# Optimization experiments

Hardware: AMD Instinct MI355X
Metric: run time of the kernel (lower is better)

The kernel has to match this reference:

```python
import jax, jax.numpy as jnp
import numpy as np

B, T, D, H = 32, 512, 512, 8
DH = D // H
NEG = -(2.0 ** 32) + 1.0  # matches torch's (-2**32 + 1) padding value
EPS = 1e-8


def setup_inputs() -> dict:
    key = jax.random.key(0)
    ks = jax.random.split(key, 10)
    s = 1.0 / np.sqrt(D)
    return {
        "queries": jax.random.normal(ks[0], (B, T, D), jnp.float32),
        "keys": jax.random.normal(ks[1], (B, T, D), jnp.float32),
        "Wq": jax.random.normal(ks[2], (D, D), jnp.float32) * s,
        "bq": jnp.zeros((D,), jnp.float32),
        "Wk": jax.random.normal(ks[3], (D, D), jnp.float32) * s,
        "bk": jnp.zeros((D,), jnp.float32),
        "Wv": jax.random.normal(ks[4], (D, D), jnp.float32) * s,
        "bv": jnp.zeros((D,), jnp.float32),
        "gamma": jnp.ones((D,), jnp.float32),
        "beta": jnp.zeros((D,), jnp.float32),
    }


def reference(queries, keys, Wq, bq, Wk, bk, Wv, bv, gamma, beta):
    b, tq, d = queries.shape
    tk = keys.shape[1]
    # projections (torch Linear: x @ W.T + b)
    Q = (queries @ Wq.T + bq).reshape(b, tq, H, DH)
    K = (keys @ Wk.T + bk).reshape(b, tk, H, DH)
    V = (keys @ Wv.T + bv).reshape(b, tk, H, DH)
    # scaled scores: [b, h, tq, tk]
    scores = jnp.einsum("bqhd,bkhd->bhqk", Q, K) / np.float32(np.sqrt(DH))
    # key padding mask (1 where key row sum != 0)
    key_mask = jnp.sign(jnp.abs(keys.sum(-1)))  # [b, tk]
    scores = jnp.where(key_mask[:, None, None, :] == 0, NEG, scores)
    # causal mask
    tril = jnp.tril(jnp.ones((tq, tk), scores.dtype))
    scores = jnp.where(tril[None, None, :, :] == 0, NEG, scores)
    attn = jax.nn.softmax(scores, axis=-1)  # [b, h, tq, tk]
    # query padding mask (zeros out rows for padded queries)
    query_mask = jnp.sign(jnp.abs(queries.sum(-1)))  # [b, tq]
    attn_m = attn * query_mask[:, None, :, None]
    # (dropout_rate == 0 -> identity)
    out = jnp.einsum("bhqk,bkhd->bqhd", attn_m, V).reshape(b, tq, d)
    # residual + LayerNorm (torch .std() is unbiased, ddof=1; eps added to std)
    x = out + queries
    mean = x.mean(-1, keepdims=True)
    std = jnp.std(x, axis=-1, ddof=1, keepdims=True)
    y = gamma * (x - mean) / (std + EPS) + beta
    return y
```

## Files before the change

kernel.cpp:

```cpp
#include <hip/hip_runtime.h>
#include <hip/hip_bf16.h>
#include <math.h>

#define B 32
#define T 512
#define D 512
#define H 8
#define DH 64
#define NEGV (-4294967295.0f)
#define LN_EPS 1e-8f

typedef __attribute__((ext_vector_type(8))) short bf16x8;
typedef __attribute__((ext_vector_type(4))) float f32x4;

__device__ inline f32x4 mfma16(bf16x8 a, bf16x8 b, f32x4 c) {
    return __builtin_amdgcn_mfma_f32_16x16x32_bf16(a, b, c, 0, 0, 0);
}

__device__ inline float fexp2(float x) { return __builtin_amdgcn_exp2f(x); }

#define GLDS16(g, l)                                                      \
    __builtin_amdgcn_global_load_lds(                                     \
        (const __attribute__((address_space(1))) void*)(g),               \
        (__attribute__((address_space(3))) void*)(l), 16, 0, 0)

__device__ inline unsigned short bf16bits(float x) {
    __hip_bfloat16 h = __float2bfloat16(x);
    union { __hip_bfloat16 h; unsigned short u; } cv;
    cv.h = h;
    return cv.u;
}

__device__ inline float b2f(unsigned short u) {
    union { unsigned u; float f; } c;
    c.u = ((unsigned)u) << 16;
    return c.f;
}

__global__ __launch_bounds__(256) void convert_all(
    const float* __restrict__ queries, const float* __restrict__ keys,
    const float* __restrict__ Wq, const float* __restrict__ Wk,
    const float* __restrict__ Wv,
    __hip_bfloat16* __restrict__ Qx, __hip_bfloat16* __restrict__ Kx,
    __hip_bfloat16* __restrict__ Wbf,
    float* __restrict__ qmask, float* __restrict__ kmask)
{
    const int tid = threadIdx.x;
    if (blockIdx.x >= 4096) {
        const int i = (blockIdx.x - 4096) * 2 + blockIdx.y;
        const int mat = i >> 7;
        const float* Ws = (mat == 0) ? Wq : (mat == 1) ? Wk : Wv;
        const int idx = ((i & 127) * 256 + tid) * 8;
        float4 a = *(const float4*)&Ws[idx];
        float4 c = *(const float4*)&Ws[idx + 4];
        union { unsigned short u[8]; bf16x8 v; } pk;
        pk.u[0] = bf16bits(a.x); pk.u[1] = bf16bits(a.y);
        pk.u[2] = bf16bits(a.z); pk.u[3] = bf16bits(a.w);
        pk.u[4] = bf16bits(c.x); pk.u[5] = bf16bits(c.y);
        pk.u[6] = bf16bits(c.z); pk.u[7] = bf16bits(c.w);
        *(bf16x8*)&Wbf[(size_t)mat * 262144 + idx] = pk.v;
        return;
    }

    const int wid = tid >> 6;
    const int lane = tid & 63;
    const int row = blockIdx.x * 4 + wid;
    const float* src = blockIdx.y ? keys : queries;
    __hip_bfloat16* dst = blockIdx.y ? Kx : Qx;
    float* dm = blockIdx.y ? kmask : qmask;

    const float4* p = (const float4*)(src + (size_t)row * 512);
    float4 a = p[lane * 2];
    float4 c = p[lane * 2 + 1];
    float s = a.x + a.y + a.z + a.w + c.x + c.y + c.z + c.w;

    union { unsigned short u[8]; bf16x8 v; } pk;
    pk.u[0] = bf16bits(a.x); pk.u[1] = bf16bits(a.y);
    pk.u[2] = bf16bits(a.z); pk.u[3] = bf16bits(a.w);
    pk.u[4] = bf16bits(c.x); pk.u[5] = bf16bits(c.y);
    pk.u[6] = bf16bits(c.z); pk.u[7] = bf16bits(c.w);
    *(bf16x8*)&dst[(size_t)row * 512 + lane * 8] = pk.v;

#pragma unroll
    for (int off = 32; off > 0; off >>= 1) s += __shfl_xor(s, off, 64);
    if (lane == 0)
        dm[row] = blockIdx.y ? ((s != 0.0f) ? 0.0f : NEGV)
                             : ((s != 0.0f) ? 1.0f : 0.0f);
}

__global__ __launch_bounds__(256) void qkv_qk(
    const __hip_bfloat16* __restrict__ Qx, const __hip_bfloat16* __restrict__ Kx,
    const __hip_bfloat16* __restrict__ Wbf,
    const float* __restrict__ bq, const float* __restrict__ bk,
    __hip_bfloat16* __restrict__ Qbf, __hip_bfloat16* __restrict__ Kbf)
{
    const int mat = blockIdx.z;
    const __hip_bfloat16* X  = mat ? Kx : Qx;
    const __hip_bfloat16* Wm = Wbf + (size_t)mat * 262144;
    const float* bias = mat ? bk : bq;
    __hip_bfloat16* Out = mat ? Kbf : Qbf;
    const float sc = mat ? 1.0f : 0.18033688011112042f;

    const int bm = blockIdx.x * 128;
    const int bn = blockIdx.y * 128;
    const int tid = threadIdx.x;
    const int w = tid >> 6, lane = tid & 63;
    const int lo = lane & 15, hi = lane >> 4;
    const int wm = (w >> 1) * 64, wn = (w & 1) * 64;

    __shared__ __hip_bfloat16 As[2][128 * 32];
    __shared__ __hip_bfloat16 Bs[2][128 * 32];

    const int r0 = tid >> 2,          g0 = (tid & 3) ^ ((r0 >> 1) & 3);
    const int r1 = (tid + 256) >> 2,  g1 = ((tid + 256) & 3) ^ ((r1 >> 1) & 3);
    const __hip_bfloat16* sA0 = X  + (size_t)(bm + r0) * 512 + g0 * 8;
    const __hip_bfloat16* sA1 = X  + (size_t)(bm + r1) * 512 + g1 * 8;
    const __hip_bfloat16* sB0 = Wm + (size_t)(bn + r0) * 512 + g0 * 8;
    const __hip_bfloat16* sB1 = Wm + (size_t)(bn + r1) * 512 + g1 * 8;
    const int dst0 = (w * 64) * 8;
    const int dst1 = (256 + w * 64) * 8;

    int offA[4], offB[4];
#pragma unroll
    for (int mi = 0; mi < 4; ++mi) {
        int r = wm + mi * 16 + lo;
        offA[mi] = r * 32 + ((hi ^ ((r >> 1) & 3)) * 8);
    }
#pragma unroll
    for (int ni = 0; ni < 4; ++ni) {
        int r = wn + ni * 16 + lo;
        offB[ni] = r * 32 + ((hi ^ ((r >> 1) & 3)) * 8);
    }

    f32x4 acc[4][4];
#pragma unroll
    for (int mi = 0; mi < 4; ++mi)
#pragma unroll
        for (int ni = 0; ni < 4; ++ni)
            acc[mi][ni] = (f32x4){0.f, 0.f, 0.f, 0.f};

    GLDS16(sA0, &As[0][dst0]);
    GLDS16(sA1, &As[0][dst1]);
    GLDS16(sB0, &Bs[0][dst0]);
    GLDS16(sB1, &Bs[0][dst1]);
    __syncthreads();

    for (int kt = 0; kt < 16; ++kt) {
        const int cur = kt & 1;
        if (kt < 15) {
            const int k0 = (kt + 1) * 32;
            GLDS16(sA0 + k0, &As[cur ^ 1][dst0]);
            GLDS16(sA1 + k0, &As[cur ^ 1][dst1]);
            GLDS16(sB0 + k0, &Bs[cur ^ 1][dst0]);
            GLDS16(sB1 + k0, &Bs[cur ^ 1][dst1]);
        }
        bf16x8 af[4], bfr[4];
#pragma unroll
        for (int mi = 0; mi < 4; ++mi) af[mi]  = *(const bf16x8*)&As[cur][offA[mi]];
#pragma unroll
        for (int ni = 0; ni < 4; ++ni) bfr[ni] = *(const bf16x8*)&Bs[cur][offB[ni]];
#pragma unroll
        for (int mi = 0; mi < 4; ++mi)
#pragma unroll
            for (int ni = 0; ni < 4; ++ni)
                acc[mi][ni] = mfma16(bfr[ni], af[mi], acc[mi][ni]);
        __syncthreads();
    }

    float4 b4[4];
#pragma unroll
    for (int ni = 0; ni < 4; ++ni)
        b4[ni] = *(const float4*)&bias[bn + wn + ni * 16 + hi * 4];
#pragma unroll
    for (int mi = 0; mi < 4; ++mi) {
        const size_t tok = bm + wm + mi * 16 + lo;
        __hip_bfloat16* orow = Out + tok * 512 + bn + wn + hi * 4;
#pragma unroll
        for (int ni = 0; ni < 4; ++ni) {
            union { ushort4 u4; unsigned short us[4]; } pk;
            pk.us[0] = bf16bits((acc[mi][ni][0] + b4[ni].x) * sc);
            pk.us[1] = bf16bits((acc[mi][ni][1] + b4[ni].y) * sc);
            pk.us[2] = bf16bits((acc[mi][ni][2] + b4[ni].z) * sc);
            pk.us[3] = bf16bits((acc[mi][ni][3] + b4[ni].w) * sc);
            *(ushort4*)(orow + ni * 16) = pk.u4;
        }
    }
}

__global__ __launch_bounds__(256) void qkv_v(
    const __hip_bfloat16* __restrict__ Kx, const __hip_bfloat16* __restrict__ Wbf,
    const float* __restrict__ bv, __hip_bfloat16* __restrict__ Vtb)
{
    const __hip_bfloat16* X  = Kx;
    const __hip_bfloat16* Wm = Wbf + (size_t)2 * 262144;
    const float* bias = bv;

    const int bm = blockIdx.x * 128;
    const int bn = blockIdx.y * 128;
    const int tid = threadIdx.x;
    const int w = tid >> 6, lane = tid & 63;
    const int lo = lane & 15, hi = lane >> 4;
    const int wm = (w >> 1) * 64, wn = (w & 1) * 64;

    __shared__ __hip_bfloat16 As[2][128 * 32];
    __shared__ __hip_bfloat16 Bs[2][128 * 32];

    const int r0 = tid >> 2,          g0 = (tid & 3) ^ ((r0 >> 1) & 3);
    const int r1 = (tid + 256) >> 2,  g1 = ((tid + 256) & 3) ^ ((r1 >> 1) & 3);
    const __hip_bfloat16* sA0 = X  + (size_t)(bm + r0) * 512 + g0 * 8;
    const __hip_bfloat16* sA1 = X  + (size_t)(bm + r1) * 512 + g1 * 8;
    const __hip_bfloat16* sB0 = Wm + (size_t)(bn + r0) * 512 + g0 * 8;
    const __hip_bfloat16* sB1 = Wm + (size_t)(bn + r1) * 512 + g1 * 8;
    const int dst0 = (w * 64) * 8;
    const int dst1 = (256 + w * 64) * 8;

    int offA[4], offB[4];
#pragma unroll
    for (int mi = 0; mi < 4; ++mi) {
        int r = wm + mi * 16 + lo;
        offA[mi] = r * 32 + ((hi ^ ((r >> 1) & 3)) * 8);
    }
#pragma unroll
    for (int ni = 0; ni < 4; ++ni) {
        int r = wn + ni * 16 + lo;
        offB[ni] = r * 32 + ((hi ^ ((r >> 1) & 3)) * 8);
    }

    f32x4 acc[4][4];
#pragma unroll
    for (int mi = 0; mi < 4; ++mi)
#pragma unroll
        for (int ni = 0; ni < 4; ++ni)
            acc[mi][ni] = (f32x4){0.f, 0.f, 0.f, 0.f};

    GLDS16(sA0, &As[0][dst0]);
    GLDS16(sA1, &As[0][dst1]);
    GLDS16(sB0, &Bs[0][dst0]);
    GLDS16(sB1, &Bs[0][dst1]);
    __syncthreads();

    for (int kt = 0; kt < 16; ++kt) {
        const int cur = kt & 1;
        if (kt < 15) {
            const int k0 = (kt + 1) * 32;
            GLDS16(sA0 + k0, &As[cur ^ 1][dst0]);
            GLDS16(sA1 + k0, &As[cur ^ 1][dst1]);
            GLDS16(sB0 + k0, &Bs[cur ^ 1][dst0]);
            GLDS16(sB1 + k0, &Bs[cur ^ 1][dst1]);
        }
        bf16x8 af[4], bfr[4];
#pragma unroll
        for (int mi = 0; mi < 4; ++mi) af[mi]  = *(const bf16x8*)&As[cur][offA[mi]];
#pragma unroll
        for (int ni = 0; ni < 4; ++ni) bfr[ni] = *(const bf16x8*)&Bs[cur][offB[ni]];
#pragma unroll
        for (int mi = 0; mi < 4; ++mi)
#pragma unroll
            for (int ni = 0; ni < 4; ++ni)
                acc[mi][ni] = mfma16(af[mi], bfr[ni], acc[mi][ni]);
        __syncthreads();
    }

    float bcol[4];
#pragma unroll
    for (int ni = 0; ni < 4; ++ni) bcol[ni] = bias[bn + wn + ni * 16 + lo];
    const int bb = bm >> 9;
    const int tb = (bm & 511) + wm;
#pragma unroll
    for (int ni = 0; ni < 4; ++ni) {
        const int n = bn + wn + ni * 16 + lo;
        const int hh = n >> 6, dh = n & 63;
#pragma unroll
        for (int mi = 0; mi < 4; ++mi) {
            const int tok = tb + mi * 16 + hi * 4;
            const int ktl = tok >> 6, tl = tok & 63;
            union { ushort4 u4; unsigned short us[4]; } pk;
#pragma unroll
            for (int j = 0; j < 4; ++j)
                pk.us[j] = bf16bits(acc[mi][ni][j] + bcol[ni]);
            *(ushort4*)(Vtb + ((((size_t)(bb * 8 + hh) * 8 + ktl) * 64 + dh) * 64 + tl))
                = pk.u4;
        }
    }
}

__global__ __launch_bounds__(256, 4) void flash_attn(
    const __hip_bfloat16* __restrict__ Qbf, const __hip_bfloat16* __restrict__ Kbf,
    const __hip_bfloat16* __restrict__ Vtb, const float* __restrict__ qmask,
    const float* __restrict__ kmneg, __hip_bfloat16* __restrict__ Oattn)
{
    const int flat = blockIdx.x + (blockIdx.y << 2) + (blockIdx.z << 5);
    const int rm = ((flat & 7) << 7) + (flat >> 3);
    const int pr = rm & 3;
    const int h  = (rm >> 2) & 7;
    const int b  = rm >> 5;

    const int tid  = threadIdx.x;
    const int w    = tid >> 6;
    const int lane = tid & 63;
    const int lo = lane & 15;
    const int hi = lane >> 4;

    __shared__ __hip_bfloat16 Ks[2][4096];
    __shared__ __hip_bfloat16 p_lds[4][16][72];

    const float* km = kmneg + b * T;
    const __hip_bfloat16* Kh = Kbf + (size_t)b * T * D + h * DH;
    const __hip_bfloat16* Vh = Vtb + (size_t)(b * H + h) * T * DH;

    const int sr0 = tid >> 3,         sg0 = (tid & 7) ^ (sr0 & 7);
    const int sr1 = (tid + 256) >> 3, sg1 = ((tid + 256) & 7) ^ (sr1 & 7);
    const __hip_bfloat16* sK0 = Kh + (size_t)sr0 * 512 + sg0 * 8;
    const __hip_bfloat16* sK1 = Kh + (size_t)sr1 * 512 + sg1 * 8;
    __hip_bfloat16* dK0a = &Ks[0][w * 512];
    __hip_bfloat16* dK0b = &Ks[0][2048 + w * 512];
    __hip_bfloat16* dK1a = &Ks[1][w * 512];
    __hip_bfloat16* dK1b = &Ks[1][2048 + w * 512];

#define STAGEK(bufp, kt) do {                                              \
        const size_t _o = (size_t)(kt) * 32768;                            \
        GLDS16(sK0 + _o, (bufp) ? dK1a : dK0a);                            \
        GLDS16(sK1 + _o, (bufp) ? dK1b : dK0b);                            \
    } while (0)

    int kfoff[4][2];
#pragma unroll
    for (int c = 0; c < 4; ++c)
#pragma unroll
        for (int j = 0; j < 2; ++j)
            kfoff[c][j] = (c * 16 + lo) * 64 + (((j * 4 + hi) ^ (lo & 7)) * 8);

    f32x4 cb[4];
#pragma unroll
    for (int c = 0; c < 4; ++c)
#pragma unroll
        for (int j = 0; j < 4; ++j)
            cb[c][j] = (c * 16 + hi * 4 + j <= w * 16 + lo) ? 0.0f : NEGV;

    const int nt1 = pr + 1;

    int qtile = pr;
    int q = qtile * 64 + w * 16 + lo;
    const __hip_bfloat16* Qrow = Qbf + (size_t)(b * T + q) * D + h * DH;
    bf16x8 qf0 = *(const bf16x8*)(Qrow + hi * 8);
    bf16x8 qf1 = *(const bf16x8*)(Qrow + 32 + hi * 8);

    f32x4 o[4];
    float mrun = -INFINITY, lrun = 0.f;
#pragma unroll
    for (int d = 0; d < 4; ++d) o[d] = (f32x4){0.f, 0.f, 0.f, 0.f};

    STAGEK(0, 0);

    for (int i = 0; i < 9; ++i) {
        const int cur = i & 1;
        const bool diag = (i == nt1 - 1) || (i == 8);
        if (i < 8) {
            const int nxt = (i + 1 < nt1) ? (i + 1) : (i + 1 - nt1);
            STAGEK(cur ^ 1, nxt);
            asm volatile("s_waitcnt vmcnt(2)" ::: "memory");
        } else {
            asm volatile("s_waitcnt vmcnt(0)" ::: "memory");
        }
        __builtin_amdgcn_s_barrier();
        __builtin_amdgcn_sched_barrier(0);

        if (i == nt1) {
            const float inv = qmask[b * T + q] / lrun;
            __hip_bfloat16* orow = Oattn + (size_t)(b * T + q) * D + h * DH;
#pragma unroll
            for (int db = 0; db < 4; ++db) {
                union { ushort4 u4; unsigned short us[4]; } pk;
#pragma unroll
                for (int j = 0; j < 4; ++j)
                    pk.us[j] = bf16bits(o[db][j] * inv);
                *(ushort4*)(orow + db * 16 + hi * 4) = pk.u4;
            }
            qtile = 7 - pr;
            q = qtile * 64 + w * 16 + lo;
            const __hip_bfloat16* Qrow2 = Qbf + (size_t)(b * T + q) * D + h * DH;
            qf0 = *(const bf16x8*)(Qrow2 + hi * 8);
            qf1 = *(const bf16x8*)(Qrow2 + 32 + hi * 8);
            mrun = -INFINITY; lrun = 0.f;
#pragma unroll
            for (int d = 0; d < 4; ++d) o[d] = (f32x4){0.f, 0.f, 0.f, 0.f};
        }

        const int kt = (i < nt1) ? i : (i - nt1);
        const int kb = kt * 64;

        const __hip_bfloat16* Vtile = Vh + (size_t)kt * 4096;
        bf16x8 vf[4][2];
#pragma unroll
        for (int db = 0; db < 4; ++db) {
            const __hip_bfloat16* Vrow = Vtile + (db * 16 + lo) * 64;
            vf[db][0] = *(const bf16x8*)(Vrow + hi * 8);
            vf[db][1] = *(const bf16x8*)(Vrow + 32 + hi * 8);
        }

        bf16x8 kf[4][2];
#pragma unroll
        for (int c = 0; c < 4; ++c) {
            kf[c][0] = *(const bf16x8*)&Ks[cur][kfoff[c][0]];
            kf[c][1] = *(const bf16x8*)&Ks[cur][kfoff[c][1]];
        }

        f32x4 S[4];
#pragma unroll
        for (int c = 0; c < 4; ++c) {
            f32x4 acc = (f32x4){0.f, 0.f, 0.f, 0.f};
            acc = mfma16(kf[c][0], qf0, acc);
            acc = mfma16(kf[c][1], qf1, acc);
            acc += *(const f32x4*)(km + kb + c * 16 + hi * 4);
            if (diag) acc += cb[c];
            S[c] = acc;
        }

        float tm0 = fmaxf(fmaxf(S[0][0], S[0][1]), fmaxf(S[0][2], S[0][3]));
        float tm1 = fmaxf(fmaxf(S[1][0], S[1][1]), fmaxf(S[1][2], S[1][3]));
        float tm2 = fmaxf(fmaxf(S[2][0], S[2][1]), fmaxf(S[2][2], S[2][3]));
        float tm3 = fmaxf(fmaxf(S[3][0], S[3][1]), fmaxf(S[3][2], S[3][3]));
        float tm = fmaxf(fmaxf(tm0, tm1), fmaxf(tm2, tm3));
        tm = fmaxf(tm, __shfl_xor(tm, 16, 64));
        tm = fmaxf(tm, __shfl_xor(tm, 32, 64));

        const float nm = fmaxf(mrun, tm);
        const float alpha = fexp2(mrun - nm);
        mrun = nm;
#pragma unroll
        for (int d = 0; d < 4; ++d)
#pragma unroll
            for (int j = 0; j < 4; ++j)
                o[d][j] *= alpha;

        float ps = 0.f;
#pragma unroll
        for (int c = 0; c < 4; ++c) {
            union { ushort4 u4; unsigned short us[4]; } pk;
#pragma unroll
            for (int j = 0; j < 4; ++j) {
                float p = fexp2(S[c][j] - nm);
                ps += p;
                pk.us[j] = bf16bits(p);
            }
            *(ushort4*)&p_lds[w][lo][c * 16 + hi * 4] = pk.u4;
        }
        ps += __shfl_xor(ps, 16, 64);
        ps += __shfl_xor(ps, 32, 64);
        lrun = lrun * alpha + ps;

        asm volatile("s_waitcnt lgkmcnt(0)" ::: "memory");
        __builtin_amdgcn_sched_barrier(0);

#pragma unroll
        for (int half = 0; half < 2; ++half) {
            bf16x8 pf = *(const bf16x8*)&p_lds[w][lo][half * 32 + hi * 8];
#pragma unroll
            for (int db = 0; db < 4; ++db)
                o[db] = mfma16(vf[db][half], pf, o[db]);
        }

        __builtin_amdgcn_s_barrier();
    }

    {
        const float inv = qmask[b * T + q] / lrun;
        __hip_bfloat16* orow = Oattn + (size_t)(b * T + q) * D + h * DH;
#pragma unroll
        for (int db = 0; db < 4; ++db) {
            union { ushort4 u4; unsigned short us[4]; } pk;
#pragma unroll
            for (int j = 0; j < 4; ++j)
                pk.us[j] = bf16bits(o[db][j] * inv);
            *(ushort4*)(orow + db * 16 + hi * 4) = pk.u4;
        }
    }
#undef STAGEK
}

__global__ __launch_bounds__(256) void resid_ln(
    const __hip_bfloat16* __restrict__ Oa, const float* __restrict__ queries,
    const float* __restrict__ gamma, const float* __restrict__ beta,
    float* __restrict__ out)
{
    const int w = threadIdx.x >> 6;
    const int lane = threadIdx.x & 63;
    const int row = blockIdx.x * 4 + w;
    const size_t base = (size_t)row * 512 + lane * 8;

    bf16x8 oa = *(const bf16x8*)((const unsigned short*)Oa + base);
    float4 q0 = *(const float4*)(queries + base);
    float4 q1 = *(const float4*)(queries + base + 4);

    float x[8];
    x[0] = b2f((unsigned short)oa[0]) + q0.x;
    x[1] = b2f((unsigned short)oa[1]) + q0.y;
    x[2] = b2f((unsigned short)oa[2]) + q0.z;
    x[3] = b2f((unsigned short)oa[3]) + q0.w;
    x[4] = b2f((unsigned short)oa[4]) + q1.x;
    x[5] = b2f((unsigned short)oa[5]) + q1.y;
    x[6] = b2f((unsigned short)oa[6]) + q1.z;
    x[7] = b2f((unsigned short)oa[7]) + q1.w;

    float s = ((x[0] + x[1]) + (x[2] + x[3])) + ((x[4] + x[5]) + (x[6] + x[7]));
#pragma unroll
    for (int off = 32; off > 0; off >>= 1) s += __shfl_xor(s, off, 64);
    const float mean = s * (1.0f / 512.0f);

    float d[8], ss = 0.f;
#pragma unroll
    for (int j = 0; j < 8; ++j) { d[j] = x[j] - mean; ss += d[j] * d[j]; }
#pragma unroll
    for (int off = 32; off > 0; off >>= 1) ss += __shfl_xor(ss, off, 64);
    const float denom = sqrtf(ss * (1.0f / 511.0f)) + LN_EPS;
    const float rden = 1.0f / denom;

    float4 g0 = *(const float4*)(gamma + lane * 8);
    float4 g1 = *(const float4*)(gamma + lane * 8 + 4);
    float4 b0 = *(const float4*)(beta + lane * 8);
    float4 b1 = *(const float4*)(beta + lane * 8 + 4);

    float4 r0, r1;
    r0.x = g0.x * d[0] * rden + b0.x;
    r0.y = g0.y * d[1] * rden + b0.y;
    r0.z = g0.z * d[2] * rden + b0.z;
    r0.w = g0.w * d[3] * rden + b0.w;
    r1.x = g1.x * d[4] * rden + b1.x;
    r1.y = g1.y * d[5] * rden + b1.y;
    r1.z = g1.z * d[6] * rden + b1.z;
    r1.w = g1.w * d[7] * rden + b1.w;
    *(float4*)(out + base) = r0;
    *(float4*)(out + base + 4) = r1;
}

extern "C" void kernel_launch(void* const* d_in, const int* in_sizes, int n_in,
                              void* d_out, int out_size, void* d_ws, size_t ws_size,
                              hipStream_t stream)
{
    const float* queries = (const float*)d_in[0];
    const float* keys    = (const float*)d_in[1];
    const float* Wq      = (const float*)d_in[2];
    const float* bq      = (const float*)d_in[3];
    const float* Wk      = (const float*)d_in[4];
    const float* bk      = (const float*)d_in[5];
    const float* Wv      = (const float*)d_in[6];
    const float* bv      = (const float*)d_in[7];
    const float* gamma   = (const float*)d_in[8];
    const float* beta    = (const float*)d_in[9];
    float* out = (float*)d_out;

    char* ws = (char*)d_ws;
    __hip_bfloat16* Qbf   = (__hip_bfloat16*)(ws);
    __hip_bfloat16* Kbf   = (__hip_bfloat16*)(ws + 16777216);
    __hip_bfloat16* Vtb   = (__hip_bfloat16*)(ws + 33554432);
    __hip_bfloat16* Qx    = (__hip_bfloat16*)(ws + 50331648);
    __hip_bfloat16* Oattn = (__hip_bfloat16*)(ws + 50331648);
    __hip_bfloat16* Kx    = (__hip_bfloat16*)(ws + 67108864);
    __hip_bfloat16* Wbf   = (__hip_bfloat16*)(ws + 83886080);
    float* qmask          = (float*)(ws + 85458944);
    float* kmask          = (float*)(ws + 85524480);

    convert_all<<<dim3(4288, 2), 256, 0, stream>>>(
        queries, keys, Wq, Wk, Wv, Qx, Kx, Wbf, qmask, kmask);
    qkv_qk<<<dim3(128, 4, 2), 256, 0, stream>>>(
        Qx, Kx, Wbf, bq, bk, Qbf, Kbf);
    qkv_v<<<dim3(128, 4), 256, 0, stream>>>(Kx, Wbf, bv, Vtb);
    flash_attn<<<dim3(4, 8, 32), 256, 0, stream>>>(
        Qbf, Kbf, Vtb, qmask, kmask, Oattn);
    resid_ln<<<4096, 256, 0, stream>>>(Oattn, queries, gamma, beta, out);
}
```

Measured before the change: 128.2 us.

## Process 128-query tiles per block with two fragments per wave in flash attention

Each flash-attention block now covers a 128-row query group (two 16-row fragments per wave) and pairs group g with group 3-g for causal load balance. Every staged K tile and every loaded V fragment is reused across twice as many queries, which halves K/V traffic per query and halves the grid. Per-wave causal skipping (kt <= tqw) avoids fully masked tiles. In exchange register use roughly doubles, the occupancy hint drops from 4 to 2 blocks, and the grid shrinks to 512 blocks.

```diff
diff --git a/kernel.cpp b/kernel.cpp
--- a/kernel.cpp
+++ b/kernel.cpp
@@ -284,16 +284,16 @@
     }
 }
 
-__global__ __launch_bounds__(256, 4) void flash_attn(
+__global__ __launch_bounds__(256, 2) void flash_attn(
     const __hip_bfloat16* __restrict__ Qbf, const __hip_bfloat16* __restrict__ Kbf,
     const __hip_bfloat16* __restrict__ Vtb, const float* __restrict__ qmask,
     const float* __restrict__ kmneg, __hip_bfloat16* __restrict__ Oattn)
 {
-    const int flat = blockIdx.x + (blockIdx.y << 2) + (blockIdx.z << 5);
-    const int rm = ((flat & 7) << 7) + (flat >> 3);
-    const int pr = rm & 3;
-    const int h  = (rm >> 2) & 7;
-    const int b  = rm >> 5;
+    const int flat = blockIdx.x + (blockIdx.y << 1) + (blockIdx.z << 4);
+    const int rm = ((flat & 7) << 6) + (flat >> 3);
+    const int pg = rm & 1;
+    const int h  = (rm >> 1) & 7;
+    const int b  = rm >> 4;
 
     const int tid  = threadIdx.x;
     const int w    = tid >> 6;
@@ -302,7 +302,7 @@
     const int hi = lane >> 4;
 
     __shared__ __hip_bfloat16 Ks[2][4096];
-    __shared__ __hip_bfloat16 p_lds[4][16][72];
+    __shared__ __hip_bfloat16 p_lds[4][2][16][72];
 
     const float* km = kmneg + b * T;
     const __hip_bfloat16* Kh = Kbf + (size_t)b * T * D + h * DH;
@@ -330,34 +330,41 @@
         for (int j = 0; j < 2; ++j)
             kfoff[c][j] = (c * 16 + lo) * 64 + (((j * 4 + hi) ^ (lo & 7)) * 8);
 
-    f32x4 cb[4];
-#pragma unroll
-    for (int c = 0; c < 4; ++c)
-#pragma unroll
-        for (int j = 0; j < 4; ++j)
-            cb[c][j] = (c * 16 + hi * 4 + j <= w * 16 + lo) ? 0.0f : NEGV;
-
-    const int nt1 = pr + 1;
-
-    int qtile = pr;
-    int q = qtile * 64 + w * 16 + lo;
-    const __hip_bfloat16* Qrow = Qbf + (size_t)(b * T + q) * D + h * DH;
-    bf16x8 qf0 = *(const bf16x8*)(Qrow + hi * 8);
-    bf16x8 qf1 = *(const bf16x8*)(Qrow + 32 + hi * 8);
-
-    f32x4 o[4];
-    float mrun = -INFINITY, lrun = 0.f;
-#pragma unroll
-    for (int d = 0; d < 4; ++d) o[d] = (f32x4){0.f, 0.f, 0.f, 0.f};
+    const int qloc0 = (32 * w + lo) & 63;
+    const int qloc1 = (32 * w + 16 + lo) & 63;
+
+    const int len1 = 2 * pg + 2;
+
+    int g = pg;
+    int tqw = 2 * g + (w >> 1);
+    int qb = g * 128 + w * 32 + lo;
+
+    bf16x8 qf[2][2];
+    {
+        const __hip_bfloat16* Q0 = Qbf + (size_t)(b * T + qb) * D + h * DH;
+        qf[0][0] = *(const bf16x8*)(Q0 + hi * 8);
+        qf[0][1] = *(const bf16x8*)(Q0 + 32 + hi * 8);
+        const __hip_bfloat16* Q1 = Q0 + (size_t)16 * D;
+        qf[1][0] = *(const bf16x8*)(Q1 + hi * 8);
+        qf[1][1] = *(const bf16x8*)(Q1 + 32 + hi * 8);
+    }
+
+    f32x4 o[2][4];
+    float mrun[2], lrun[2];
+#pragma unroll
+    for (int f = 0; f < 2; ++f) {
+        mrun[f] = -INFINITY; lrun[f] = 0.f;
+#pragma unroll
+        for (int d = 0; d < 4; ++d) o[f][d] = (f32x4){0.f, 0.f, 0.f, 0.f};
+    }
 
     STAGEK(0, 0);
 
-    for (int i = 0; i < 9; ++i) {
+    for (int i = 0; i < 10; ++i) {
         const int cur = i & 1;
-        const bool diag = (i == nt1 - 1) || (i == 8);
-        if (i < 8) {
-            const int nxt = (i + 1 < nt1) ? (i + 1) : (i + 1 - nt1);
-            STAGEK(cur ^ 1, nxt);
+        if (i < 9) {
+            const int nkt = (i + 1 < len1) ? (i + 1) : (i + 1 - len1);
+            STAGEK(cur ^ 1, nkt);
             asm volatile("s_waitcnt vmcnt(2)" ::: "memory");
         } else {
             asm volatile("s_waitcnt vmcnt(0)" ::: "memory");
@@ -365,113 +372,146 @@
         __builtin_amdgcn_s_barrier();
         __builtin_amdgcn_sched_barrier(0);
 
-        if (i == nt1) {
-            const float inv = qmask[b * T + q] / lrun;
-            __hip_bfloat16* orow = Oattn + (size_t)(b * T + q) * D + h * DH;
+        if (i == len1) {
+#pragma unroll
+            for (int f = 0; f < 2; ++f) {
+                const int qr = qb + f * 16;
+                const float inv = qmask[b * T + qr] / lrun[f];
+                __hip_bfloat16* orow = Oattn + (size_t)(b * T + qr) * D + h * DH;
+#pragma unroll
+                for (int db = 0; db < 4; ++db) {
+                    union { ushort4 u4; unsigned short us[4]; } pk;
+#pragma unroll
+                    for (int j = 0; j < 4; ++j)
+                        pk.us[j] = bf16bits(o[f][db][j] * inv);
+                    *(ushort4*)(orow + db * 16 + hi * 4) = pk.u4;
+                }
+            }
+            g = 3 - pg;
+            tqw = 2 * g + (w >> 1);
+            qb = g * 128 + w * 32 + lo;
+            const __hip_bfloat16* Q0 = Qbf + (size_t)(b * T + qb) * D + h * DH;
+            qf[0][0] = *(const bf16x8*)(Q0 + hi * 8);
+            qf[0][1] = *(const bf16x8*)(Q0 + 32 + hi * 8);
+            const __hip_bfloat16* Q1 = Q0 + (size_t)16 * D;
+            qf[1][0] = *(const bf16x8*)(Q1 + hi * 8);
+            qf[1][1] = *(const bf16x8*)(Q1 + 32 + hi * 8);
+#pragma unroll
+            for (int f = 0; f < 2; ++f) {
+                mrun[f] = -INFINITY; lrun[f] = 0.f;
+#pragma unroll
+                for (int d = 0; d < 4; ++d) o[f][d] = (f32x4){0.f, 0.f, 0.f, 0.f};
+            }
+        }
+
+        const int kt = (i < len1) ? i : (i - len1);
+
+        if (kt <= tqw) {
+            const int kb = kt * 64;
+            const bool diag = (kt == tqw);
+
+            f32x4 kmb[4];
+#pragma unroll
+            for (int c = 0; c < 4; ++c)
+                kmb[c] = *(const f32x4*)(km + kb + c * 16 + hi * 4);
+
+            const __hip_bfloat16* Vtile = Vh + (size_t)kt * 4096;
+            bf16x8 vf[4][2];
 #pragma unroll
             for (int db = 0; db < 4; ++db) {
-                union { ushort4 u4; unsigned short us[4]; } pk;
-#pragma unroll
-                for (int j = 0; j < 4; ++j)
-                    pk.us[j] = bf16bits(o[db][j] * inv);
-                *(ushort4*)(orow + db * 16 + hi * 4) = pk.u4;
+                const __hip_bfloat16* Vrow = Vtile + (db * 16 + lo) * 64;
+                vf[db][0] = *(const bf16x8*)(Vrow + hi * 8);
+                vf[db][1] = *(const bf16x8*)(Vrow + 32 + hi * 8);
             }
-            qtile = 7 - pr;
-            q = qtile * 64 + w * 16 + lo;
-            const __hip_bfloat16* Qrow2 = Qbf + (size_t)(b * T + q) * D + h * DH;
-            qf0 = *(const bf16x8*)(Qrow2 + hi * 8);
-            qf1 = *(const bf16x8*)(Qrow2 + 32 + hi * 8);
-            mrun = -INFINITY; lrun = 0.f;
-#pragma unroll
-            for (int d = 0; d < 4; ++d) o[d] = (f32x4){0.f, 0.f, 0.f, 0.f};
-        }
-
-        const int kt = (i < nt1) ? i : (i - nt1);
-        const int kb = kt * 64;
-
-        const __hip_bfloat16* Vtile = Vh + (size_t)kt * 4096;
-        bf16x8 vf[4][2];
-#pragma unroll
-        for (int db = 0; db < 4; ++db) {
-            const __hip_bfloat16* Vrow = Vtile + (db * 16 + lo) * 64;
-            vf[db][0] = *(const bf16x8*)(Vrow + hi * 8);
-            vf[db][1] = *(const bf16x8*)(Vrow + 32 + hi * 8);
-        }
-
-        bf16x8 kf[4][2];
-#pragma unroll
-        for (int c = 0; c < 4; ++c) {
-            kf[c][0] = *(const bf16x8*)&Ks[cur][kfoff[c][0]];
-            kf[c][1] = *(const bf16x8*)&Ks[cur][kfoff[c][1]];
-        }
-
-        f32x4 S[4];
-#pragma unroll
-        for (int c = 0; c < 4; ++c) {
-            f32x4 acc = (f32x4){0.f, 0.f, 0.f, 0.f};
-            acc = mfma16(kf[c][0], qf0, acc);
-            acc = mfma16(kf[c][1], qf1, acc);
-            acc += *(const f32x4*)(km + kb + c * 16 + hi * 4);
-            if (diag) acc += cb[c];
-            S[c] = acc;
-        }
-
-        float tm0 = fmaxf(fmaxf(S[0][0], S[0][1]), fmaxf(S[0][2], S[0][3]));
-        float tm1 = fmaxf(fmaxf(S[1][0], S[1][1]), fmaxf(S[1][2], S[1][3]));
-        float tm2 = fmaxf(fmaxf(S[2][0], S[2][1]), fmaxf(S[2][2], S[2][3]));
-        float tm3 = fmaxf(fmaxf(S[3][0], S[3][1]), fmaxf(S[3][2], S[3][3]));
-        float tm = fmaxf(fmaxf(tm0, tm1), fmaxf(tm2, tm3));
-        tm = fmaxf(tm, __shfl_xor(tm, 16, 64));
-        tm = fmaxf(tm, __shfl_xor(tm, 32, 64));
-
-        const float nm = fmaxf(mrun, tm);
-        const float alpha = fexp2(mrun - nm);
-        mrun = nm;
-#pragma unroll
-        for (int d = 0; d < 4; ++d)
-#pragma unroll
-            for (int j = 0; j < 4; ++j)
-                o[d][j] *= alpha;
-
-        float ps = 0.f;
-#pragma unroll
-        for (int c = 0; c < 4; ++c) {
-            union { ushort4 u4; unsigned short us[4]; } pk;
-#pragma unroll
-            for (int j = 0; j < 4; ++j) {
-                float p = fexp2(S[c][j] - nm);
-                ps += p;
-                pk.us[j] = bf16bits(p);
+
+            bf16x8 kf[4][2];
+#pragma unroll
+            for (int c = 0; c < 4; ++c) {
+                kf[c][0] = *(const bf16x8*)&Ks[cur][kfoff[c][0]];
+                kf[c][1] = *(const bf16x8*)&Ks[cur][kfoff[c][1]];
             }
-            *(ushort4*)&p_lds[w][lo][c * 16 + hi * 4] = pk.u4;
-        }
-        ps += __shfl_xor(ps, 16, 64);
-        ps += __shfl_xor(ps, 32, 64);
-        lrun = lrun * alpha + ps;
-
-        asm volatile("s_waitcnt lgkmcnt(0)" ::: "memory");
-        __builtin_amdgcn_sched_barrier(0);
-
-#pragma unroll
-        for (int half = 0; half < 2; ++half) {
-            bf16x8 pf = *(const bf16x8*)&p_lds[w][lo][half * 32 + hi * 8];
-#pragma unroll
-            for (int db = 0; db < 4; ++db)
-                o[db] = mfma16(vf[db][half], pf, o[db]);
+
+#pragma unroll
+            for (int f = 0; f < 2; ++f) {
+                const int qloc = f ? qloc1 : qloc0;
+                f32x4 S[4];
+#pragma unroll
+                for (int c = 0; c < 4; ++c) {
+                    f32x4 acc = (f32x4){0.f, 0.f, 0.f, 0.f};
+                    acc = mfma16(kf[c][0], qf[f][0], acc);
+                    acc = mfma16(kf[c][1], qf[f][1], acc);
+                    acc += kmb[c];
+                    if (diag) {
+#pragma unroll
+                        for (int j = 0; j < 4; ++j)
+                            acc[j] = (c * 16 + hi * 4 + j <= qloc) ? acc[j] : NEGV;
+                    }
+                    S[c] = acc;
+                }
+
+                float tm0 = fmaxf(fmaxf(S[0][0], S[0][1]), fmaxf(S[0][2], S[0][3]));
+                float tm1 = fmaxf(fmaxf(S[1][0], S[1][1]), fmaxf(S[1][2], S[1][3]));
+                float tm2 = fmaxf(fmaxf(S[2][0], S[2][1]), fmaxf(S[2][2], S[2][3]));
+                float tm3 = fmaxf(fmaxf(S[3][0], S[3][1]), fmaxf(S[3][2], S[3][3]));
+                float tm = fmaxf(fmaxf(tm0, tm1), fmaxf(tm2, tm3));
+                tm = fmaxf(tm, __shfl_xor(tm, 16, 64));
+                tm = fmaxf(tm, __shfl_xor(tm, 32, 64));
+
+                const float nm = fmaxf(mrun[f], tm);
+                const float alpha = fexp2(mrun[f] - nm);
+                mrun[f] = nm;
+#pragma unroll
+                for (int d = 0; d < 4; ++d)
+#pragma unroll
+                    for (int j = 0; j < 4; ++j)
+                        o[f][d][j] *= alpha;
+
+                float ps = 0.f;
+#pragma unroll
+                for (int c = 0; c < 4; ++c) {
+                    union { ushort4 u4; unsigned short us[4]; } pk;
+#pragma unroll
+                    for (int j = 0; j < 4; ++j) {
+                        float p = fexp2(S[c][j] - nm);
+                        ps += p;
+                        pk.us[j] = bf16bits(p);
+                    }
+                    *(ushort4*)&p_lds[w][f][lo][c * 16 + hi * 4] = pk.u4;
+                }
+                ps += __shfl_xor(ps, 16, 64);
+                ps += __shfl_xor(ps, 32, 64);
+                lrun[f] = lrun[f] * alpha + ps;
+            }
+
+            asm volatile("s_waitcnt lgkmcnt(0)" ::: "memory");
+            __builtin_amdgcn_sched_barrier(0);
+
+#pragma unroll
+            for (int half = 0; half < 2; ++half) {
+                bf16x8 pf0 = *(const bf16x8*)&p_lds[w][0][lo][half * 32 + hi * 8];
+                bf16x8 pf1 = *(const bf16x8*)&p_lds[w][1][lo][half * 32 + hi * 8];
+#pragma unroll
+                for (int db = 0; db < 4; ++db) {
+                    o[0][db] = mfma16(vf[db][half], pf0, o[0][db]);
+                    o[1][db] = mfma16(vf[db][half], pf1, o[1][db]);
+                }
+            }
         }
 
         __builtin_amdgcn_s_barrier();
     }
 
-    {
-        const float inv = qmask[b * T + q] / lrun;
-        __hip_bfloat16* orow = Oattn + (size_t)(b * T + q) * D + h * DH;
+#pragma unroll
+    for (int f = 0; f < 2; ++f) {
+        const int qr = qb + f * 16;
+        const float inv = qmask[b * T + qr] / lrun[f];
+        __hip_bfloat16* orow = Oattn + (size_t)(b * T + qr) * D + h * DH;
 #pragma unroll
         for (int db = 0; db < 4; ++db) {
             union { ushort4 u4; unsigned short us[4]; } pk;
 #pragma unroll
             for (int j = 0; j < 4; ++j)
-                pk.us[j] = bf16bits(o[db][j] * inv);
+                pk.us[j] = bf16bits(o[f][db][j] * inv);
             *(ushort4*)(orow + db * 16 + hi * 4) = pk.u4;
         }
     }
@@ -565,7 +605,7 @@
     qkv_qk<<<dim3(128, 4, 2), 256, 0, stream>>>(
         Qx, Kx, Wbf, bq, bk, Qbf, Kbf);
     qkv_v<<<dim3(128, 4), 256, 0, stream>>>(Kx, Wbf, bv, Vtb);
-    flash_attn<<<dim3(4, 8, 32), 256, 0, stream>>>(
+    flash_attn<<<dim3(2, 8, 32), 256, 0, stream>>>(
         Qbf, Kbf, Vtb, qmask, kmask, Oattn);
     resid_ln<<<4096, 256, 0, stream>>>(Oattn, queries, gamma, beta, out);
 }
```

Result: faster. 113.4 us (median of 2 runs) (-11.5%).
